# Kernel tuning notes

Hardware: AMD Instinct MI355X
Metric: run time of the kernel (lower is better)

The kernel has to match this reference:

```python
import jax, jax.numpy as jnp
import numpy as np

CHANNELS = 96


def make_sharpen_kernel(channels: int) -> jnp.ndarray:
    # (C_out, C_in, 3, 3), block-diagonal: per-channel 3x3 sharpen stencil
    k = jnp.full((3, 3), -0.1, dtype=jnp.float32).at[1, 1].set(1.8)
    eye = jnp.eye(channels, dtype=jnp.float32)  # (C, C)
    return eye[:, :, None, None] * k[None, None, :, :]


def setup_inputs() -> dict:
    key = jax.random.key(0)
    x = jax.random.normal(key, (16, CHANNELS, 256, 256), dtype=jnp.float32)
    kernel = make_sharpen_kernel(CHANNELS)
    return {"x": x, "kernel": kernel}


def reference(x, kernel):
    # Faithful to F.conv2d(x, kernel, stride=1, padding=1) with the dense
    # (block-diagonal) kernel the torch module constructs.
    return jax.lax.conv_general_dilated(
        x, kernel,
        window_strides=(1, 1),
        padding=((1, 1), (1, 1)),
        dimension_numbers=("NCHW", "OIHW", "NCHW"),
    )
```

## Files before the change

kernel.cpp:

```cpp
#include <hip/hip_runtime.h>

#define CHN 96
#define IMG_H 256
#define IMG_W 256
#define STRIP 64
#define WPB 8

typedef float vfloat4 __attribute__((ext_vector_type(4)));

struct Row { float l, x, y, z, w, r; };

__device__ __forceinline__ Row mkrow(vfloat4 v, int lane) {
    Row r;
    r.x = v.x; r.y = v.y; r.z = v.z; r.w = v.w;
    r.l = __shfl_up(v.w, 1);
    r.r = __shfl_down(v.x, 1);
    if (lane == 0)  r.l = 0.f;
    if (lane == 63) r.r = 0.f;
    return r;
}

__device__ __forceinline__ vfloat4 stencil(const Row& a, const Row& b, const Row& c,
                                           float w0, float w1, float w2,
                                           float w3, float w4, float w5,
                                           float w6, float w7, float w8) {
    vfloat4 o;
    o.x = w0*a.l + w1*a.x + w2*a.y
        + w3*b.l + w4*b.x + w5*b.y
        + w6*c.l + w7*c.x + w8*c.y;
    o.y = w0*a.x + w1*a.y + w2*a.z
        + w3*b.x + w4*b.y + w5*b.z
        + w6*c.x + w7*c.y + w8*c.z;
    o.z = w0*a.y + w1*a.z + w2*a.w
        + w3*b.y + w4*b.z + w5*b.w
        + w6*c.y + w7*c.z + w8*c.w;
    o.w = w0*a.z + w1*a.w + w2*a.r
        + w3*b.z + w4*b.w + w5*b.r
        + w6*c.z + w7*c.w + w8*c.r;
    return o;
}

__global__ __launch_bounds__(WPB * 64)
void sharpen3x3_strip(const float* __restrict__ x,
                      const float* __restrict__ kern,
                      float* __restrict__ out)
{
    const int lane = threadIdx.x & 63;
    const int wave = threadIdx.x >> 6;

    const int strip_id = blockIdx.x * WPB + wave;
    const int spp      = IMG_H / STRIP;
    const int plane    = strip_id / spp;
    const int sy       = (strip_id % spp) * STRIP;
    const int c        = plane % CHN;

    const float* kw = kern + ((size_t)c * CHN + c) * 9;
    const float w0 = kw[0], w1 = kw[1], w2 = kw[2];
    const float w3 = kw[3], w4 = kw[4], w5 = kw[5];
    const float w6 = kw[6], w7 = kw[7], w8 = kw[8];

    const float* xp = x   + (size_t)plane * IMG_H * IMG_W;
    float*       op = out + (size_t)plane * IMG_H * IMG_W;

    const int col = 4 * lane;

    Row prev, cur;
    if (sy == 0) {
        prev = Row{0.f, 0.f, 0.f, 0.f, 0.f, 0.f};
    } else {
        vfloat4 vp = *(const vfloat4*)(xp + (size_t)(sy - 1) * IMG_W + col);
        prev = mkrow(vp, lane);
    }
    {
        vfloat4 vc = *(const vfloat4*)(xp + (size_t)sy * IMG_W + col);
        cur = mkrow(vc, lane);
    }

    for (int i = 0; i < STRIP; i += 4) {
        const int y = sy + i;
        const float* base = xp + (size_t)(y + 1) * IMG_W + col;

        vfloat4 v0 = *(const vfloat4*)(base);
        vfloat4 v1 = *(const vfloat4*)(base + IMG_W);
        vfloat4 v2 = *(const vfloat4*)(base + 2 * IMG_W);
        vfloat4 v3;
        const bool last = (y + 4 >= IMG_H);
        if (!last) v3 = *(const vfloat4*)(base + 3 * IMG_W);
        else       v3 = (vfloat4){0.f, 0.f, 0.f, 0.f};

        Row n0 = mkrow(v0, lane);
        Row n1 = mkrow(v1, lane);
        Row n2 = mkrow(v2, lane);
        Row n3 = last ? Row{0.f,0.f,0.f,0.f,0.f,0.f} : mkrow(v3, lane);

        vfloat4 o0 = stencil(prev, cur, n0, w0,w1,w2,w3,w4,w5,w6,w7,w8);
        vfloat4 o1 = stencil(cur,  n0,  n1, w0,w1,w2,w3,w4,w5,w6,w7,w8);
        vfloat4 o2 = stencil(n0,   n1,  n2, w0,w1,w2,w3,w4,w5,w6,w7,w8);
        vfloat4 o3 = stencil(n1,   n2,  n3, w0,w1,w2,w3,w4,w5,w6,w7,w8);

        float* ob = op + (size_t)y * IMG_W + col;
        __builtin_nontemporal_store(o0, (vfloat4*)(ob));
        __builtin_nontemporal_store(o1, (vfloat4*)(ob + IMG_W));
        __builtin_nontemporal_store(o2, (vfloat4*)(ob + 2 * IMG_W));
        __builtin_nontemporal_store(o3, (vfloat4*)(ob + 3 * IMG_W));

        prev = n2;
        cur  = n3;
    }
}

extern "C" void kernel_launch(void* const* d_in, const int* in_sizes, int n_in,
                              void* d_out, int out_size, void* d_ws, size_t ws_size,
                              hipStream_t stream) {
    const float* x    = (const float*)d_in[0];
    const float* kern = (const float*)d_in[1];
    float* out        = (float*)d_out;

    const int n_strips = 16 * CHN * (IMG_H / STRIP);
    const int grid     = n_strips / WPB;

    hipLaunchKernelGGL(sharpen3x3_strip, dim3(grid), dim3(WPB * 64),
                       0, stream, x, kern, out);
}
```

Baseline: 158.9 us.

## Software-pipeline strip rows with register double-buffering and nontemporal loads

Restructures the per-wave strip loop so each group of 8 input rows is prefetched into registers one iteration ahead, while the current group is run through the stencil one row at a time. Input loads also become nontemporal, and out-of-image rows are zero-filled through a bounds-checked load helper. The aim is to keep more memory requests in flight per wave and hide load latency in a bandwidth-bound kernel. In exchange it raises register use, which may lower occupancy, and the kernel is already close to memory bandwidth, leaving little room.

```diff
diff --git a/kernel.cpp b/kernel.cpp
--- a/kernel.cpp
+++ b/kernel.cpp
@@ -5,6 +5,7 @@
 #define IMG_W 256
 #define STRIP 64
 #define WPB 8
+#define GRP 8
 
 typedef float vfloat4 __attribute__((ext_vector_type(4)));
 
@@ -18,6 +19,13 @@
     if (lane == 0)  r.l = 0.f;
     if (lane == 63) r.r = 0.f;
     return r;
+}
+
+__device__ __forceinline__ vfloat4 ldrow(const float* xp, int yy, int col) {
+    if (yy < IMG_H)
+        return __builtin_nontemporal_load(
+            (const vfloat4*)(xp + (size_t)yy * IMG_W + col));
+    return (vfloat4){0.f, 0.f, 0.f, 0.f};
 }
 
 __device__ __forceinline__ vfloat4 stencil(const Row& a, const Row& b, const Row& c,
@@ -41,9 +49,9 @@
 }
 
 __global__ __launch_bounds__(WPB * 64)
-void sharpen3x3_strip(const float* __restrict__ x,
-                      const float* __restrict__ kern,
-                      float* __restrict__ out)
+void sharpen3x3_pipe(const float* __restrict__ x,
+                     const float* __restrict__ kern,
+                     float* __restrict__ out)
 {
     const int lane = threadIdx.x & 63;
     const int wave = threadIdx.x >> 6;
@@ -68,44 +76,42 @@
     if (sy == 0) {
         prev = Row{0.f, 0.f, 0.f, 0.f, 0.f, 0.f};
     } else {
-        vfloat4 vp = *(const vfloat4*)(xp + (size_t)(sy - 1) * IMG_W + col);
-        prev = mkrow(vp, lane);
+        prev = mkrow(ldrow(xp, sy - 1, col), lane);
     }
-    {
-        vfloat4 vc = *(const vfloat4*)(xp + (size_t)sy * IMG_W + col);
-        cur = mkrow(vc, lane);
-    }
+    cur = mkrow(ldrow(xp, sy, col), lane);
 
-    for (int i = 0; i < STRIP; i += 4) {
-        const int y = sy + i;
-        const float* base = xp + (size_t)(y + 1) * IMG_W + col;
+    vfloat4 va[GRP];
+    #pragma unroll
+    for (int j = 0; j < GRP; ++j) va[j] = ldrow(xp, sy + 1 + j, col);
 
-        vfloat4 v0 = *(const vfloat4*)(base);
-        vfloat4 v1 = *(const vfloat4*)(base + IMG_W);
-        vfloat4 v2 = *(const vfloat4*)(base + 2 * IMG_W);
-        vfloat4 v3;
-        const bool last = (y + 4 >= IMG_H);
-        if (!last) v3 = *(const vfloat4*)(base + 3 * IMG_W);
-        else       v3 = (vfloat4){0.f, 0.f, 0.f, 0.f};
+    #pragma unroll 1
+    for (int g = 0; g < STRIP / GRP; ++g) {
+        const int y = sy + g * GRP;
 
-        Row n0 = mkrow(v0, lane);
-        Row n1 = mkrow(v1, lane);
-        Row n2 = mkrow(v2, lane);
-        Row n3 = last ? Row{0.f,0.f,0.f,0.f,0.f,0.f} : mkrow(v3, lane);
+        vfloat4 vb[GRP];
+        if (g + 1 < STRIP / GRP) {
+            #pragma unroll
+            for (int j = 0; j < GRP; ++j)
+                vb[j] = ldrow(xp, y + GRP + 1 + j, col);
+        } else {
+            #pragma unroll
+            for (int j = 0; j < GRP; ++j)
+                vb[j] = (vfloat4){0.f, 0.f, 0.f, 0.f};
+        }
 
-        vfloat4 o0 = stencil(prev, cur, n0, w0,w1,w2,w3,w4,w5,w6,w7,w8);
-        vfloat4 o1 = stencil(cur,  n0,  n1, w0,w1,w2,w3,w4,w5,w6,w7,w8);
-        vfloat4 o2 = stencil(n0,   n1,  n2, w0,w1,w2,w3,w4,w5,w6,w7,w8);
-        vfloat4 o3 = stencil(n1,   n2,  n3, w0,w1,w2,w3,w4,w5,w6,w7,w8);
+        #pragma unroll
+        for (int j = 0; j < GRP; ++j) {
+            Row n = mkrow(va[j], lane);
+            vfloat4 o = stencil(prev, cur, n,
+                                w0,w1,w2,w3,w4,w5,w6,w7,w8);
+            __builtin_nontemporal_store(
+                o, (vfloat4*)(op + (size_t)(y + j) * IMG_W + col));
+            prev = cur;
+            cur  = n;
+        }
 
-        float* ob = op + (size_t)y * IMG_W + col;
-        __builtin_nontemporal_store(o0, (vfloat4*)(ob));
-        __builtin_nontemporal_store(o1, (vfloat4*)(ob + IMG_W));
-        __builtin_nontemporal_store(o2, (vfloat4*)(ob + 2 * IMG_W));
-        __builtin_nontemporal_store(o3, (vfloat4*)(ob + 3 * IMG_W));
-
-        prev = n2;
-        cur  = n3;
+        #pragma unroll
+        for (int j = 0; j < GRP; ++j) va[j] = vb[j];
     }
 }
 
@@ -119,6 +125,6 @@
     const int n_strips = 16 * CHN * (IMG_H / STRIP);
     const int grid     = n_strips / WPB;
 
-    hipLaunchKernelGGL(sharpen3x3_strip, dim3(grid), dim3(WPB * 64),
+    hipLaunchKernelGGL(sharpen3x3_pipe, dim3(grid), dim3(WPB * 64),
                        0, stream, x, kern, out);
 }
```

Result: faster. 153.8 us (-3.2%).
